# Kernel optimization log

Measured on AMD Instinct MI355X. Metric: run time of the kernel, lower is better.

The kernel has to match this reference:

```python
import jax, jax.numpy as jnp
import numpy as np

K = 20          # num neighbors (init kwarg k)
BN_EPS = 1e-5   # PyTorch BatchNorm default eps


def setup_inputs() -> dict:
    key = jax.random.key(0)
    k1, k2 = jax.random.split(key, 2)
    x = jax.random.normal(k1, (8, 64, 4096), dtype=jnp.float32)       # (b, d, n)
    w = jax.random.normal(k2, (64, 128), dtype=jnp.float32) * 0.05    # Conv2d 1x1: (out=64, in=2*64)
    gamma = jnp.ones((64,), jnp.float32)    # BatchNorm1d weight
    beta = jnp.zeros((64,), jnp.float32)    # BatchNorm1d bias
    return {"x": x, "w": w, "gamma": gamma, "beta": beta}


def reference(x, w, gamma, beta):
    # x: (b, d, n)
    xt = jnp.swapaxes(x, 1, 2)                       # (b, n, d)
    # kNN via pairwise squared euclidean distance (same ordering as torch.cdist)
    sq = jnp.sum(xt * xt, axis=-1)                   # (b, n)
    d2 = sq[:, :, None] + sq[:, None, :] - 2.0 * jnp.einsum('bnd,bmd->bnm', xt, xt)
    _, idx = jax.lax.top_k(-d2, K)                   # (b, n, K) smallest distances
    # gather neighbor features: (b, n, K, d)
    nb = jax.vmap(lambda pts, i: pts[i])(xt, idx)
    ctr = xt[:, :, None, :]                          # (b, n, 1, d)
    # edge feature = concat([neighbor - x, x]) -> (b, n, K, 2d)
    feat = jnp.concatenate([nb - ctr, jnp.broadcast_to(ctr, nb.shape)], axis=-1)
    # 1x1 conv (no bias) then max over neighbors
    h = jnp.max(jnp.einsum('bnkc,oc->bnko', feat, w), axis=2)   # (b, n, out)
    # BatchNorm1d (training mode: batch statistics over (b, n), biased var)
    mean = jnp.mean(h, axis=(0, 1))
    var = jnp.mean((h - mean) ** 2, axis=(0, 1))
    hn = (h - mean) / jnp.sqrt(var + BN_EPS) * gamma + beta
    out = jax.nn.gelu(hn, approximate=False)         # exact GELU (PyTorch default)
    return jnp.swapaxes(out, 1, 2)                   # (b, out, n)
```

## Files before the change

### kernel.cpp

```cpp
#include <hip/hip_runtime.h>

#define BIGF 3.402823466e38f

typedef __attribute__((ext_vector_type(8))) short bf16x8;
typedef __attribute__((ext_vector_type(4))) float f32x4;

__device__ __forceinline__ void gload_lds16(const float* g, float* lds) {
  __builtin_amdgcn_global_load_lds((const __attribute__((address_space(1))) void*)g,
                                   (__attribute__((address_space(3))) void*)lds, 16, 0, 0);
}
__device__ __forceinline__ void gload_lds16u(const unsigned short* g, unsigned short* lds) {
  __builtin_amdgcn_global_load_lds((const __attribute__((address_space(1))) void*)g,
                                   (__attribute__((address_space(3))) void*)lds, 16, 0, 0);
}

__device__ __forceinline__ unsigned short bf16_rne(float f) {
  unsigned int u = __float_as_uint(f);
  return (unsigned short)((u + 0x7fffu + ((u >> 16) & 1u)) >> 16);
}

__global__ __launch_bounds__(256) void k1_pre(const float* __restrict__ x, const float* __restrict__ w,
                                              float* __restrict__ sq, float* __restrict__ y,
                                              float* __restrict__ delta, unsigned short* __restrict__ xhl) {
  __shared__ __align__(16) float xt[64][68];
  __shared__ __align__(16) float ws[128][64];
  const int t = threadIdx.x;
  const int bid = blockIdx.x;
  const int b = bid >> 6;
  const int n0 = (bid & 63) << 6;
  const float* xb = x + (size_t)b * 64 * 4096;

#pragma unroll
  for (int rep = 0; rep < 16; ++rep) {
    int id = rep * 256 + t;
    int d = id >> 6, n = id & 63;
    xt[n][d] = xb[(size_t)d * 4096 + n0 + n];
  }
#pragma unroll
  for (int rep = 0; rep < 32; ++rep) {
    int id = rep * 256 + t;
    int u = id >> 6, dd = id & 63;
    ws[u][dd] = w[(u & 63) * 128 + ((u >> 6) << 6) + dd];
  }
  __syncthreads();

  {
    const int p = t >> 2;
    const int cg = t & 3;
    uint4* orow = (uint4*)xhl + ((size_t)(b << 12) + n0 + p) * 16;
#pragma unroll
    for (int cc = 0; cc < 4; ++cc) {
      const int c = cg * 4 + cc;
      const int kb = (c & 7) * 8;
      const bool lohalf = (c >= 8);
      unsigned int pk[4];
#pragma unroll
      for (int j2 = 0; j2 < 4; ++j2) {
        unsigned short u0, u1;
#pragma unroll
        for (int e = 0; e < 2; ++e) {
          const float xv = xt[p][kb + j2 * 2 + e];
          unsigned short h = bf16_rne(xv);
          unsigned short r;
          if (!lohalf) r = h;
          else r = bf16_rne(xv - __uint_as_float(((unsigned int)h) << 16));
          if (e == 0) u0 = r; else u1 = r;
        }
        pk[j2] = (unsigned int)u0 | ((unsigned int)u1 << 16);
      }
      uint4 v;
      v.x = pk[0]; v.y = pk[1]; v.z = pk[2]; v.w = pk[3];
      orow[c ^ (p & 7)] = v;
    }
  }

  const int p = t & 63;
  const int oc = t >> 6;
  float accy[16], accz[16];
#pragma unroll
  for (int j = 0; j < 16; ++j) { accy[j] = 0.f; accz[j] = 0.f; }

#pragma unroll 4
  for (int d4 = 0; d4 < 16; ++d4) {
    const float4 xv = *(const float4*)&xt[p][d4 * 4];
#pragma unroll
    for (int j = 0; j < 16; ++j) {
      const int o = oc * 16 + j;
      const float4 wy = *(const float4*)&ws[o][d4 * 4];
      const float4 wz = *(const float4*)&ws[o + 64][d4 * 4];
      accy[j] = fmaf(xv.x, wy.x, fmaf(xv.y, wy.y, fmaf(xv.z, wy.z, fmaf(xv.w, wy.w, accy[j]))));
      accz[j] = fmaf(xv.x, wz.x, fmaf(xv.y, wz.y, fmaf(xv.z, wz.z, fmaf(xv.w, wz.w, accz[j]))));
    }
  }

  if (oc == 0) {
    float s = 0.f;
#pragma unroll
    for (int d4 = 0; d4 < 16; ++d4) {
      const float4 v = *(const float4*)&xt[p][d4 * 4];
      s = fmaf(v.x, v.x, fmaf(v.y, v.y, fmaf(v.z, v.z, fmaf(v.w, v.w, s))));
    }
    sq[b * 4096 + n0 + p] = s;
  }

  const size_t row = ((size_t)b * 4096 + n0 + p) * 64 + oc * 16;
#pragma unroll
  for (int j4 = 0; j4 < 4; ++j4) {
    float4 yv = make_float4(accy[j4 * 4], accy[j4 * 4 + 1], accy[j4 * 4 + 2], accy[j4 * 4 + 3]);
    float4 dv = make_float4(accz[j4 * 4] - accy[j4 * 4], accz[j4 * 4 + 1] - accy[j4 * 4 + 1],
                            accz[j4 * 4 + 2] - accy[j4 * 4 + 2], accz[j4 * 4 + 3] - accy[j4 * 4 + 3]);
    *(float4*)&y[row + j4 * 4] = yv;
    *(float4*)&delta[row + j4 * 4] = dv;
  }
}

__global__ __launch_bounds__(256, 2) void k2_knn(const unsigned short* __restrict__ xhl,
                                                 const float* __restrict__ sq,
                                                 int* __restrict__ idx_out) {
  __shared__ __align__(16) float smem[4096 + 8192 + 6656];
  const int t = threadIdx.x;
  const int lane = t & 63;
  const int w = t >> 6;
  float* BsW = smem + 4096 + (w << 11);
  uint4* BsW4 = (uint4*)BsW;
  const uint4* As4 = (const uint4*)smem;
  uint2* bufL = (uint2*)(smem + 12288) + ((w << 6) + lane) * 13;

  const int bid = blockIdx.x;
  const int b = bid >> 6;
  const int n0 = (bid & 63) << 6;
  const int pn = lane & 15, q = lane >> 4;

  const unsigned short* xr = xhl + ((size_t)(b << 12)) * 128;
  const float* sqb = sq + (b << 12);

  {
    unsigned short* asu = (unsigned short*)smem;
#pragma unroll
    for (int qq = 0; qq < 4; ++qq) {
      const int kk = w * 4 + qq;
      gload_lds16u(xr + (size_t)n0 * 128 + kk * 512 + lane * 8, asu + kk * 512);
    }
  }
  __syncthreads();

  bf16x8 bfr[4][4];
#pragma unroll
  for (int nt = 0; nt < 4; ++nt)
#pragma unroll
    for (int j = 0; j < 4; ++j)
      bfr[nt][j] = *reinterpret_cast<const bf16x8*>(&As4[((nt << 4) + pn) * 16 + (((j << 2) + q) ^ (pn & 7))]);

  float kd[20];
  int ki[20];
#pragma unroll
  for (int s = 0; s < 20; ++s) { kd[s] = BIGF; ki[s] = -1; }
  const float sqn = sqb[n0 + lane];
  const int myn = lane;
  const int swz = myn & 7;
  int cnt = 0;

  auto ins = [&](float vd, int vi) {
#pragma unroll
    for (int s = 0; s < 20; ++s) {
      const float od = kd[s];
      const int oi = ki[s];
      const bool lt = vd < od;
      kd[s] = lt ? vd : od;
      ki[s] = lt ? vi : oi;
      vd = lt ? od : vd;
      vi = lt ? oi : vi;
    }
  };

  auto drain = [&]() {
#pragma unroll 1
    for (int j = 0; j < 12; ++j) {
      if (!__any(j < cnt)) break;
      if (j < cnt) {
        const uint2 e = bufL[j];
        const float dv = __uint_as_float(e.x);
        if (dv < kd[19]) ins(dv, (int)e.y);
      }
    }
    cnt = 0;
  };

  const f32x4 zero4 = {0.f, 0.f, 0.f, 0.f};
  f32x4 acc[4][2];
#pragma unroll
  for (int nt = 0; nt < 4; ++nt) { acc[nt][0] = zero4; acc[nt][1] = zero4; }

  for (int kt = 0; kt < 32; ++kt) {
    const int mbase = (w + 4 * kt) << 5;
    {
      unsigned short* bsu = (unsigned short*)BsW;
      const unsigned short* src = xr + (size_t)mbase * 128;
#pragma unroll
      for (int k = 0; k < 8; ++k) gload_lds16u(src + k * 512 + lane * 8, bsu + k * 512);
    }
    const f32x4 sqm0 = *(const f32x4*)&sqb[mbase + (q << 2)];
    const f32x4 sqm1 = *(const f32x4*)&sqb[mbase + 16 + (q << 2)];
    __builtin_amdgcn_s_waitcnt(0x0F70);

#pragma unroll
    for (int mt = 0; mt < 2; ++mt) {
      bf16x8 afr[4];
#pragma unroll
      for (int j = 0; j < 4; ++j)
        afr[j] = *reinterpret_cast<const bf16x8*>(&BsW4[((mt << 4) + pn) * 16 + (((j << 2) + q) ^ (pn & 7))]);
#pragma unroll
      for (int nt = 0; nt < 4; ++nt) {
        f32x4 a = acc[nt][mt];
        a = __builtin_amdgcn_mfma_f32_16x16x32_bf16(afr[0], bfr[nt][0], a, 0, 0, 0);
        a = __builtin_amdgcn_mfma_f32_16x16x32_bf16(afr[1], bfr[nt][1], a, 0, 0, 0);
        a = __builtin_amdgcn_mfma_f32_16x16x32_bf16(afr[0], bfr[nt][2], a, 0, 0, 0);
        a = __builtin_amdgcn_mfma_f32_16x16x32_bf16(afr[1], bfr[nt][3], a, 0, 0, 0);
        a = __builtin_amdgcn_mfma_f32_16x16x32_bf16(afr[2], bfr[nt][0], a, 0, 0, 0);
        a = __builtin_amdgcn_mfma_f32_16x16x32_bf16(afr[3], bfr[nt][1], a, 0, 0, 0);
        acc[nt][mt] = a;
      }
    }

#pragma unroll
    for (int nt = 0; nt < 4; ++nt) {
#pragma unroll
      for (int mt = 0; mt < 2; ++mt) {
        const int n = (nt << 4) + pn;
        const int g = (mt << 2) + q;
        const int pc = g ^ (n & 7);
        const f32x4 sv = mt ? sqm1 : sqm0;
        f32x4 dv = sv - 2.0f * acc[nt][mt];
        *(f32x4*)&BsW[(n << 5) + (pc << 2)] = dv;
        acc[nt][mt] = zero4;
      }
    }

#pragma unroll 1
    for (int cc = 0; cc < 8; ++cc) {
      const float4 v = *(const float4*)&BsW[(myn << 5) + ((cc ^ swz) << 2)];
      const int mb = mbase + (cc << 2);
      const float c0 = sqn + v.x, c1 = sqn + v.y, c2 = sqn + v.z, c3 = sqn + v.w;
      const float thr = kd[19];
      const float mn = fminf(fminf(c0, c1), fminf(c2, c3));
      if (mn < thr) {
        if (c0 < thr) { bufL[cnt] = make_uint2(__float_as_uint(c0), (unsigned)mb); cnt++; }
        if (c1 < thr) { bufL[cnt] = make_uint2(__float_as_uint(c1), (unsigned)(mb + 1)); cnt++; }
        if (c2 < thr) { bufL[cnt] = make_uint2(__float_as_uint(c2), (unsigned)(mb + 2)); cnt++; }
        if (c3 < thr) { bufL[cnt] = make_uint2(__float_as_uint(c3), (unsigned)(mb + 3)); cnt++; }
      }
      if (__any(cnt > 8)) drain();
    }
  }
  drain();

  __syncthreads();
  float* pf = smem;
  int* pi = (int*)(smem + 5120);
#pragma unroll
  for (int s = 0; s < 20; ++s) {
    pf[(w * 20 + s) * 64 + lane] = kd[s];
    pi[(w * 20 + s) * 64 + lane] = ki[s];
  }
  __syncthreads();
  if (w == 0) {
    auto insTie = [&](float vd, int vi) {
#pragma unroll
      for (int s = 0; s < 20; ++s) {
        const float od = kd[s];
        const int oi = ki[s];
        const bool lt = (vd < od) || (vd == od && vi < oi);
        kd[s] = lt ? vd : od;
        ki[s] = lt ? vi : oi;
        vd = lt ? od : vd;
        vi = lt ? oi : vi;
      }
    };
    for (int ww = 1; ww < 4; ++ww) {
#pragma unroll 1
      for (int s = 0; s < 20; ++s) {
        const float dv = pf[(ww * 20 + s) * 64 + lane];
        const int iv = pi[(ww * 20 + s) * 64 + lane];
        if (dv < kd[19] || (dv == kd[19] && iv < ki[19])) insTie(dv, iv);
      }
    }
    int* orow = idx_out + ((size_t)(b << 12) + n0 + lane) * 20;
#pragma unroll
    for (int s = 0; s < 20; ++s) orow[s] = ki[s];
  }
}

__global__ __launch_bounds__(256) void k3_gather(const float* __restrict__ y,
                                                 const float* __restrict__ delta,
                                                 const int* __restrict__ idx,
                                                 float* __restrict__ h,
                                                 float* __restrict__ sums,
                                                 float* __restrict__ sumsq) {
  const int t = threadIdx.x;
  const int lane = t & 63;
  const int w = t >> 6;
  const int blk = blockIdx.x;
  float s1 = 0.f, s2 = 0.f;
  for (int p = 0; p < 16; ++p) {
    const int ng = blk * 64 + w * 16 + p;
    const int b = ng >> 12;
    const int* row = idx + (size_t)ng * 20;
    float mx = -BIGF;
#pragma unroll
    for (int kk = 0; kk < 20; ++kk) {
      const int nbr = row[kk];
      mx = fmaxf(mx, y[((size_t)(b << 12) + nbr) * 64 + lane]);
    }
    const float hv = mx + delta[(size_t)ng * 64 + lane];
    h[(size_t)ng * 64 + lane] = hv;
    s1 += hv;
    s2 += hv * hv;
  }
  __shared__ float r1[4][64], r2[4][64];
  r1[w][lane] = s1;
  r2[w][lane] = s2;
  __syncthreads();
  if (w == 0) {
    const float a = r1[0][lane] + r1[1][lane] + r1[2][lane] + r1[3][lane];
    const float c = r2[0][lane] + r2[1][lane] + r2[2][lane] + r2[3][lane];
    atomicAdd(&sums[lane], a);
    atomicAdd(&sumsq[lane], c);
  }
}

__global__ __launch_bounds__(256) void k4_bn(const float* __restrict__ h,
                                             const float* __restrict__ sums,
                                             const float* __restrict__ sumsq,
                                             const float* __restrict__ gamma,
                                             const float* __restrict__ beta,
                                             float* __restrict__ out) {
  __shared__ float tile[64][65];
  const int bid = blockIdx.x;
  const int b = bid >> 6;
  const int n0 = (bid & 63) << 6;
  const int t = threadIdx.x;
  const int o = t & 63;
#pragma unroll
  for (int it = 0; it < 16; ++it) {
    const int n = (t >> 6) * 16 + it;
    tile[n][o] = h[(((size_t)b << 12) + n0 + n) * 64 + o];
  }
  __syncthreads();
  const int j = t & 63;
#pragma unroll
  for (int it = 0; it < 16; ++it) {
    const int oo = (t >> 6) * 16 + it;
    const float mean = sums[oo] * (1.0f / 32768.0f);
    const float var = sumsq[oo] * (1.0f / 32768.0f) - mean * mean;
    const float sc = gamma[oo] / sqrtf(var + 1e-5f);
    const float hv = tile[j][oo];
    const float hn = (hv - mean) * sc + beta[oo];
    const float g = 0.5f * hn * (1.0f + erff(hn * 0.70710678118654752f));
    out[((size_t)(b * 64 + oo)) * 4096 + n0 + j] = g;
  }
}

extern "C" void kernel_launch(void* const* d_in, const int* in_sizes, int n_in,
                              void* d_out, int out_size, void* d_ws, size_t ws_size,
                              hipStream_t stream) {
  const float* x = (const float*)d_in[0];
  const float* w = (const float*)d_in[1];
  const float* gamma = (const float*)d_in[2];
  const float* beta = (const float*)d_in[3];
  float* out = (float*)d_out;

  float* sq_ws = (float*)d_ws;
  float* y_ws = sq_ws + 32768;
  float* delta_ws = y_ws + 2097152;
  float* h_ws = delta_ws + 2097152;
  int* idx_ws = (int*)(h_ws + 2097152);
  float* sums = (float*)(idx_ws + 655360);
  float* sumsq = sums + 64;
  unsigned short* xhl = (unsigned short*)h_ws;

  hipMemsetAsync(sums, 0, 2 * 64 * sizeof(float), stream);
  k1_pre<<<512, 256, 0, stream>>>(x, w, sq_ws, y_ws, delta_ws, xhl);
  k2_knn<<<512, 256, 0, stream>>>(xhl, sq_ws, idx_ws);
  k3_gather<<<512, 256, 0, stream>>>(y_ws, delta_ws, idx_ws, h_ws, sums, sumsq);
  k4_bn<<<512, 256, 0, stream>>>(h_ws, sums, sumsq, gamma, beta, out);
}
```

Before: 346.6 us.

## Share per-query kNN thresholds across waves and hoist candidate filter loads

Each wave publishes its current 20th-best distance per query point to shared memory after draining. At each tile the waves read all four thresholds and filter candidates against the minimum plus a margin, so fewer candidates are pushed into the buffer and insertion-sorted. The filter now compares raw LDS values against a precomputed threshold minus the query norm, and the four float4 loads for each half are issued together. The cost is extra LDS traffic through volatile accesses, and the cross-wave reads are unsynchronised, so a wave may see a stale threshold.

```diff
diff --git a/kernel.cpp b/kernel.cpp
--- a/kernel.cpp
+++ b/kernel.cpp
@@ -117,7 +117,7 @@
 __global__ __launch_bounds__(256, 2) void k2_knn(const unsigned short* __restrict__ xhl,
                                                  const float* __restrict__ sq,
                                                  int* __restrict__ idx_out) {
-  __shared__ __align__(16) float smem[4096 + 8192 + 6656];
+  __shared__ __align__(16) float smem[4096 + 8192 + 6656 + 256];
   const int t = threadIdx.x;
   const int lane = t & 63;
   const int w = t >> 6;
@@ -125,6 +125,7 @@
   uint4* BsW4 = (uint4*)BsW;
   const uint4* As4 = (const uint4*)smem;
   uint2* bufL = (uint2*)(smem + 12288) + ((w << 6) + lane) * 13;
+  volatile float* thrW = smem + 18944;
 
   const int bid = blockIdx.x;
   const int b = bid >> 6;
@@ -133,6 +134,8 @@
 
   const unsigned short* xr = xhl + ((size_t)(b << 12)) * 128;
   const float* sqb = sq + (b << 12);
+
+  thrW[t] = BIGF;
 
   {
     unsigned short* asu = (unsigned short*)smem;
@@ -184,6 +187,7 @@
       }
     }
     cnt = 0;
+    thrW[(myn << 2) + w] = kd[19];
   };
 
   const f32x4 zero4 = {0.f, 0.f, 0.f, 0.f};
@@ -201,6 +205,15 @@
     }
     const f32x4 sqm0 = *(const f32x4*)&sqb[mbase + (q << 2)];
     const f32x4 sqm1 = *(const f32x4*)&sqb[mbase + 16 + (q << 2)];
+
+    const float tw0 = thrW[(myn << 2) + 0];
+    const float tw1 = thrW[(myn << 2) + 1];
+    const float tw2 = thrW[(myn << 2) + 2];
+    const float tw3 = thrW[(myn << 2) + 3];
+    float thrS = fminf(fminf(tw0, tw1), fminf(tw2, tw3));
+    thrS = fminf(thrS, kd[19]);
+    const float thr2 = (thrS - sqn) + 0.0625f;
+
     __builtin_amdgcn_s_waitcnt(0x0F70);
 
 #pragma unroll
@@ -237,19 +250,25 @@
     }
 
 #pragma unroll 1
-    for (int cc = 0; cc < 8; ++cc) {
-      const float4 v = *(const float4*)&BsW[(myn << 5) + ((cc ^ swz) << 2)];
-      const int mb = mbase + (cc << 2);
-      const float c0 = sqn + v.x, c1 = sqn + v.y, c2 = sqn + v.z, c3 = sqn + v.w;
-      const float thr = kd[19];
-      const float mn = fminf(fminf(c0, c1), fminf(c2, c3));
-      if (mn < thr) {
-        if (c0 < thr) { bufL[cnt] = make_uint2(__float_as_uint(c0), (unsigned)mb); cnt++; }
-        if (c1 < thr) { bufL[cnt] = make_uint2(__float_as_uint(c1), (unsigned)(mb + 1)); cnt++; }
-        if (c2 < thr) { bufL[cnt] = make_uint2(__float_as_uint(c2), (unsigned)(mb + 2)); cnt++; }
-        if (c3 < thr) { bufL[cnt] = make_uint2(__float_as_uint(c3), (unsigned)(mb + 3)); cnt++; }
-      }
-      if (__any(cnt > 8)) drain();
+    for (int half = 0; half < 2; ++half) {
+      const int cb = half << 2;
+      const float4 v0 = *(const float4*)&BsW[(myn << 5) + (((cb + 0) ^ swz) << 2)];
+      const float4 v1 = *(const float4*)&BsW[(myn << 5) + (((cb + 1) ^ swz) << 2)];
+      const float4 v2 = *(const float4*)&BsW[(myn << 5) + (((cb + 2) ^ swz) << 2)];
+      const float4 v3 = *(const float4*)&BsW[(myn << 5) + (((cb + 3) ^ swz) << 2)];
+#pragma unroll
+      for (int cc = 0; cc < 4; ++cc) {
+        const float4 v = (cc == 0) ? v0 : (cc == 1) ? v1 : (cc == 2) ? v2 : v3;
+        const int mb = mbase + ((cb + cc) << 2);
+        const float mn = fminf(fminf(v.x, v.y), fminf(v.z, v.w));
+        if (mn < thr2) {
+          if (v.x < thr2) { bufL[cnt] = make_uint2(__float_as_uint(sqn + v.x), (unsigned)mb); cnt++; }
+          if (v.y < thr2) { bufL[cnt] = make_uint2(__float_as_uint(sqn + v.y), (unsigned)(mb + 1)); cnt++; }
+          if (v.z < thr2) { bufL[cnt] = make_uint2(__float_as_uint(sqn + v.z), (unsigned)(mb + 2)); cnt++; }
+          if (v.w < thr2) { bufL[cnt] = make_uint2(__float_as_uint(sqn + v.w), (unsigned)(mb + 3)); cnt++; }
+        }
+        if (__any(cnt > 8)) drain();
+      }
     }
   }
   drain();
```

New measurement: 344.2 us. No clear change (-0.7%).

## Retile kNN kernel to 32 queries per block with shared threshold and prefetch

Applied to the files above, without the earlier changes.

The kNN kernel now processes 32 query points per block instead of 64, launching 1024 blocks at up to 3 blocks per CU with a smaller LDS footprint. Each candidate tile is 16 points, loaded asynchronously one iteration ahead. Two lanes split candidates per query and then merge. A per-query threshold in shared memory, lowered by atomicMin, lets all waves prune candidates early. The threshold test is done before adding sqn, with a small 0.0625 margin. This trades higher occupancy and pruning for smaller MFMA tiles, more atomics, and a larger final merge.

```diff
diff --git a/kernel.cpp b/kernel.cpp
--- a/kernel.cpp
+++ b/kernel.cpp
@@ -5,10 +5,6 @@
 typedef __attribute__((ext_vector_type(8))) short bf16x8;
 typedef __attribute__((ext_vector_type(4))) float f32x4;
 
-__device__ __forceinline__ void gload_lds16(const float* g, float* lds) {
-  __builtin_amdgcn_global_load_lds((const __attribute__((address_space(1))) void*)g,
-                                   (__attribute__((address_space(3))) void*)lds, 16, 0, 0);
-}
 __device__ __forceinline__ void gload_lds16u(const unsigned short* g, unsigned short* lds) {
   __builtin_amdgcn_global_load_lds((const __attribute__((address_space(1))) void*)g,
                                    (__attribute__((address_space(3))) void*)lds, 16, 0, 0);
@@ -114,50 +110,65 @@
   }
 }
 
-__global__ __launch_bounds__(256, 2) void k2_knn(const unsigned short* __restrict__ xhl,
+__global__ __launch_bounds__(256, 3) void k2_knn(const unsigned short* __restrict__ xhl,
                                                  const float* __restrict__ sq,
                                                  int* __restrict__ idx_out) {
-  __shared__ __align__(16) float smem[4096 + 8192 + 6656];
+  __shared__ __align__(16) float smem[10784];
   const int t = threadIdx.x;
   const int lane = t & 63;
   const int w = t >> 6;
-  float* BsW = smem + 4096 + (w << 11);
-  uint4* BsW4 = (uint4*)BsW;
+  const int bid = blockIdx.x;
+  const int b = bid & 7;
+  const int n0 = (bid >> 3) << 5;
+  const int pn = lane & 15, q = lane >> 4;
+  const int myn = lane & 31;
+  const int h = lane >> 5;
+
+  float* dumpW = smem + (w << 9);
+  float* stW = smem + 2048 + (w << 10);
   const uint4* As4 = (const uint4*)smem;
-  uint2* bufL = (uint2*)(smem + 12288) + ((w << 6) + lane) * 13;
-
-  const int bid = blockIdx.x;
-  const int b = bid >> 6;
-  const int n0 = (bid & 63) << 6;
-  const int pn = lane & 15, q = lane >> 4;
+  const uint4* St4 = (const uint4*)stW;
+  uint2* bufL = (uint2*)(smem + 6144) + t * 9;
+  unsigned* thrNa = (unsigned*)(smem + 10752);
+  volatile unsigned* thrNv = (volatile unsigned*)(smem + 10752);
 
   const unsigned short* xr = xhl + ((size_t)(b << 12)) * 128;
   const float* sqb = sq + (b << 12);
 
+  if (t < 32) thrNa[t] = __float_as_uint(BIGF);
+
   {
     unsigned short* asu = (unsigned short*)smem;
 #pragma unroll
-    for (int qq = 0; qq < 4; ++qq) {
-      const int kk = w * 4 + qq;
+    for (int qq = 0; qq < 2; ++qq) {
+      const int kk = (w << 1) + qq;
       gload_lds16u(xr + (size_t)n0 * 128 + kk * 512 + lane * 8, asu + kk * 512);
     }
   }
-  __syncthreads();
-
-  bf16x8 bfr[4][4];
-#pragma unroll
-  for (int nt = 0; nt < 4; ++nt)
+  {
+    unsigned short* stu = (unsigned short*)stW;
+    const unsigned short* src = xr + (size_t)(w << 4) * 128;
+#pragma unroll
+    for (int k = 0; k < 4; ++k) gload_lds16u(src + k * 512 + lane * 8, stu + k * 512);
+  }
+  f32x4 sqm = *(const f32x4*)&sqb[(w << 4) + (q << 2)];
+  __builtin_amdgcn_s_waitcnt(0x0F70);
+  __syncthreads();
+
+  bf16x8 bfr[2][4];
+#pragma unroll
+  for (int nt = 0; nt < 2; ++nt)
 #pragma unroll
     for (int j = 0; j < 4; ++j)
       bfr[nt][j] = *reinterpret_cast<const bf16x8*>(&As4[((nt << 4) + pn) * 16 + (((j << 2) + q) ^ (pn & 7))]);
+  __syncthreads();
 
   float kd[20];
   int ki[20];
 #pragma unroll
   for (int s = 0; s < 20; ++s) { kd[s] = BIGF; ki[s] = -1; }
-  const float sqn = sqb[n0 + lane];
-  const int myn = lane;
-  const int swz = myn & 7;
+  const float sqn = sqb[n0 + myn];
+  const int fdw = (myn >> 1) & 3;
   int cnt = 0;
 
   auto ins = [&](float vd, int vi) {
@@ -175,7 +186,7 @@
 
   auto drain = [&]() {
 #pragma unroll 1
-    for (int j = 0; j < 12; ++j) {
+    for (int j = 0; j < 8; ++j) {
       if (!__any(j < cnt)) break;
       if (j < cnt) {
         const uint2 e = bufL[j];
@@ -184,73 +195,74 @@
       }
     }
     cnt = 0;
+    atomicMin(&thrNa[myn], __float_as_uint(kd[19]));
   };
 
   const f32x4 zero4 = {0.f, 0.f, 0.f, 0.f};
-  f32x4 acc[4][2];
-#pragma unroll
-  for (int nt = 0; nt < 4; ++nt) { acc[nt][0] = zero4; acc[nt][1] = zero4; }
-
-  for (int kt = 0; kt < 32; ++kt) {
-    const int mbase = (w + 4 * kt) << 5;
-    {
-      unsigned short* bsu = (unsigned short*)BsW;
-      const unsigned short* src = xr + (size_t)mbase * 128;
-#pragma unroll
-      for (int k = 0; k < 8; ++k) gload_lds16u(src + k * 512 + lane * 8, bsu + k * 512);
-    }
-    const f32x4 sqm0 = *(const f32x4*)&sqb[mbase + (q << 2)];
-    const f32x4 sqm1 = *(const f32x4*)&sqb[mbase + 16 + (q << 2)];
+  f32x4 acc[2];
+  acc[0] = zero4; acc[1] = zero4;
+  f32x4 sqmN = zero4;
+
+  for (int kt = 0; kt < 64; ++kt) {
+    const int mbase = (w + (kt << 2)) << 4;
     __builtin_amdgcn_s_waitcnt(0x0F70);
 
-#pragma unroll
-    for (int mt = 0; mt < 2; ++mt) {
-      bf16x8 afr[4];
-#pragma unroll
-      for (int j = 0; j < 4; ++j)
-        afr[j] = *reinterpret_cast<const bf16x8*>(&BsW4[((mt << 4) + pn) * 16 + (((j << 2) + q) ^ (pn & 7))]);
-#pragma unroll
-      for (int nt = 0; nt < 4; ++nt) {
-        f32x4 a = acc[nt][mt];
-        a = __builtin_amdgcn_mfma_f32_16x16x32_bf16(afr[0], bfr[nt][0], a, 0, 0, 0);
-        a = __builtin_amdgcn_mfma_f32_16x16x32_bf16(afr[1], bfr[nt][1], a, 0, 0, 0);
-        a = __builtin_amdgcn_mfma_f32_16x16x32_bf16(afr[0], bfr[nt][2], a, 0, 0, 0);
-        a = __builtin_amdgcn_mfma_f32_16x16x32_bf16(afr[1], bfr[nt][3], a, 0, 0, 0);
-        a = __builtin_amdgcn_mfma_f32_16x16x32_bf16(afr[2], bfr[nt][0], a, 0, 0, 0);
-        a = __builtin_amdgcn_mfma_f32_16x16x32_bf16(afr[3], bfr[nt][1], a, 0, 0, 0);
-        acc[nt][mt] = a;
+    const float thrSh = __uint_as_float(thrNv[myn]);
+    const float thrS = fminf(thrSh, kd[19]);
+    const float thr2 = (thrS - sqn) + 0.0625f;
+
+    bf16x8 afr[4];
+#pragma unroll
+    for (int j = 0; j < 4; ++j)
+      afr[j] = *reinterpret_cast<const bf16x8*>(&St4[pn * 16 + (((j << 2) + q) ^ (pn & 7))]);
+    __builtin_amdgcn_s_waitcnt(0xC07F);
+
+    if (kt < 63) {
+      const int mbn = (w + ((kt + 1) << 2)) << 4;
+      unsigned short* stu = (unsigned short*)stW;
+      const unsigned short* src = xr + (size_t)mbn * 128;
+#pragma unroll
+      for (int k = 0; k < 4; ++k) gload_lds16u(src + k * 512 + lane * 8, stu + k * 512);
+      sqmN = *(const f32x4*)&sqb[mbn + (q << 2)];
+    }
+
+#pragma unroll
+    for (int nt = 0; nt < 2; ++nt) {
+      f32x4 a = acc[nt];
+      a = __builtin_amdgcn_mfma_f32_16x16x32_bf16(afr[0], bfr[nt][0], a, 0, 0, 0);
+      a = __builtin_amdgcn_mfma_f32_16x16x32_bf16(afr[1], bfr[nt][1], a, 0, 0, 0);
+      a = __builtin_amdgcn_mfma_f32_16x16x32_bf16(afr[0], bfr[nt][2], a, 0, 0, 0);
+      a = __builtin_amdgcn_mfma_f32_16x16x32_bf16(afr[1], bfr[nt][3], a, 0, 0, 0);
+      a = __builtin_amdgcn_mfma_f32_16x16x32_bf16(afr[2], bfr[nt][0], a, 0, 0, 0);
+      a = __builtin_amdgcn_mfma_f32_16x16x32_bf16(afr[3], bfr[nt][1], a, 0, 0, 0);
+      acc[nt] = a;
+    }
+
+#pragma unroll
+    for (int nt = 0; nt < 2; ++nt) {
+      const int n = (nt << 4) + pn;
+      const int pc = q ^ ((n >> 1) & 3);
+      f32x4 dv = sqm - 2.0f * acc[nt];
+      *(f32x4*)&dumpW[(n << 4) + (pc << 2)] = dv;
+      acc[nt] = zero4;
+    }
+
+#pragma unroll 1
+    for (int cc2 = 0; cc2 < 2; ++cc2) {
+      const int cc = (h << 1) + cc2;
+      const int pc = cc ^ fdw;
+      const float4 v = *(const float4*)&dumpW[(myn << 4) + (pc << 2)];
+      const int mb = mbase + (cc << 2);
+      const float mn = fminf(fminf(v.x, v.y), fminf(v.z, v.w));
+      if (mn < thr2) {
+        if (v.x < thr2) { bufL[cnt] = make_uint2(__float_as_uint(sqn + v.x), (unsigned)mb); cnt++; }
+        if (v.y < thr2) { bufL[cnt] = make_uint2(__float_as_uint(sqn + v.y), (unsigned)(mb + 1)); cnt++; }
+        if (v.z < thr2) { bufL[cnt] = make_uint2(__float_as_uint(sqn + v.z), (unsigned)(mb + 2)); cnt++; }
+        if (v.w < thr2) { bufL[cnt] = make_uint2(__float_as_uint(sqn + v.w), (unsigned)(mb + 3)); cnt++; }
       }
-    }
-
-#pragma unroll
-    for (int nt = 0; nt < 4; ++nt) {
-#pragma unroll
-      for (int mt = 0; mt < 2; ++mt) {
-        const int n = (nt << 4) + pn;
-        const int g = (mt << 2) + q;
-        const int pc = g ^ (n & 7);
-        const f32x4 sv = mt ? sqm1 : sqm0;
-        f32x4 dv = sv - 2.0f * acc[nt][mt];
-        *(f32x4*)&BsW[(n << 5) + (pc << 2)] = dv;
-        acc[nt][mt] = zero4;
-      }
-    }
-
-#pragma unroll 1
-    for (int cc = 0; cc < 8; ++cc) {
-      const float4 v = *(const float4*)&BsW[(myn << 5) + ((cc ^ swz) << 2)];
-      const int mb = mbase + (cc << 2);
-      const float c0 = sqn + v.x, c1 = sqn + v.y, c2 = sqn + v.z, c3 = sqn + v.w;
-      const float thr = kd[19];
-      const float mn = fminf(fminf(c0, c1), fminf(c2, c3));
-      if (mn < thr) {
-        if (c0 < thr) { bufL[cnt] = make_uint2(__float_as_uint(c0), (unsigned)mb); cnt++; }
-        if (c1 < thr) { bufL[cnt] = make_uint2(__float_as_uint(c1), (unsigned)(mb + 1)); cnt++; }
-        if (c2 < thr) { bufL[cnt] = make_uint2(__float_as_uint(c2), (unsigned)(mb + 2)); cnt++; }
-        if (c3 < thr) { bufL[cnt] = make_uint2(__float_as_uint(c3), (unsigned)(mb + 3)); cnt++; }
-      }
-      if (__any(cnt > 8)) drain();
-    }
+      if (__any(cnt > 4)) drain();
+    }
+    sqm = sqmN;
   }
   drain();
 
@@ -263,7 +275,7 @@
     pi[(w * 20 + s) * 64 + lane] = ki[s];
   }
   __syncthreads();
-  if (w == 0) {
+  if (w == 0 && lane < 32) {
     auto insTie = [&](float vd, int vi) {
 #pragma unroll
       for (int s = 0; s < 20; ++s) {
@@ -276,15 +288,19 @@
         vi = lt ? oi : vi;
       }
     };
-    for (int ww = 1; ww < 4; ++ww) {
+    for (int ww = 0; ww < 4; ++ww) {
 #pragma unroll 1
-      for (int s = 0; s < 20; ++s) {
-        const float dv = pf[(ww * 20 + s) * 64 + lane];
-        const int iv = pi[(ww * 20 + s) * 64 + lane];
-        if (dv < kd[19] || (dv == kd[19] && iv < ki[19])) insTie(dv, iv);
+      for (int hh = 0; hh < 2; ++hh) {
+        if (ww == 0 && hh == 0) continue;
+#pragma unroll 1
+        for (int s = 0; s < 20; ++s) {
+          const float dv = pf[(ww * 20 + s) * 64 + (hh << 5) + myn];
+          const int iv = pi[(ww * 20 + s) * 64 + (hh << 5) + myn];
+          if (dv < kd[19] || (dv == kd[19] && iv < ki[19])) insTie(dv, iv);
+        }
       }
     }
-    int* orow = idx_out + ((size_t)(b << 12) + n0 + lane) * 20;
+    int* orow = idx_out + ((size_t)(b << 12) + n0 + myn) * 20;
 #pragma unroll
     for (int s = 0; s < 20; ++s) orow[s] = ki[s];
   }
@@ -380,7 +396,7 @@
 
   hipMemsetAsync(sums, 0, 2 * 64 * sizeof(float), stream);
   k1_pre<<<512, 256, 0, stream>>>(x, w, sq_ws, y_ws, delta_ws, xhl);
-  k2_knn<<<512, 256, 0, stream>>>(xhl, sq_ws, idx_ws);
+  k2_knn<<<1024, 256, 0, stream>>>(xhl, sq_ws, idx_ws);
   k3_gather<<<512, 256, 0, stream>>>(y_ws, delta_ws, idx_ws, h_ws, sums, sumsq);
   k4_bn<<<512, 256, 0, stream>>>(h_ws, sums, sumsq, gamma, beta, out);
 }
```

Measured after the change: 504.0 us. 1.45x slower.

## Prefetch next kNN tile, share per-query threshold across waves, shrink candidate buffers

Applied to the files above, without the earlier changes.

Restructures the kNN distance loop so the next key tile and its squared norms are loaded into LDS while the current tile's MFMA and selection run. A per-query threshold shared across the four waves, kept in LDS and tightened with atomicMin after each drain, is used so fewer candidates pass the filter. The candidate buffer moves to a struct-of-arrays layout in reused LDS, and the dump tile is halved to 16 columns per half-tile. Risks include extra LDS atomics, a slack margin of 0.0625 on the threshold, and a subtle race in reusing the A-tile LDS region for the buffers, which is guarded by an added barrier.

```diff
diff --git a/kernel.cpp b/kernel.cpp
--- a/kernel.cpp
+++ b/kernel.cpp
@@ -5,10 +5,6 @@
 typedef __attribute__((ext_vector_type(8))) short bf16x8;
 typedef __attribute__((ext_vector_type(4))) float f32x4;
 
-__device__ __forceinline__ void gload_lds16(const float* g, float* lds) {
-  __builtin_amdgcn_global_load_lds((const __attribute__((address_space(1))) void*)g,
-                                   (__attribute__((address_space(3))) void*)lds, 16, 0, 0);
-}
 __device__ __forceinline__ void gload_lds16u(const unsigned short* g, unsigned short* lds) {
   __builtin_amdgcn_global_load_lds((const __attribute__((address_space(1))) void*)g,
                                    (__attribute__((address_space(3))) void*)lds, 16, 0, 0);
@@ -117,31 +113,46 @@
 __global__ __launch_bounds__(256, 2) void k2_knn(const unsigned short* __restrict__ xhl,
                                                  const float* __restrict__ sq,
                                                  int* __restrict__ idx_out) {
-  __shared__ __align__(16) float smem[4096 + 8192 + 6656];
+  __shared__ __align__(16) float smem[16448];
   const int t = threadIdx.x;
   const int lane = t & 63;
   const int w = t >> 6;
-  float* BsW = smem + 4096 + (w << 11);
-  uint4* BsW4 = (uint4*)BsW;
+  float* stW = smem + 4096 + (w << 11);
+  float* dumpW = smem + 12288 + (w << 10);
   const uint4* As4 = (const uint4*)smem;
-  uint2* bufL = (uint2*)(smem + 12288) + ((w << 6) + lane) * 13;
+  const uint4* St4 = (const uint4*)stW;
+  unsigned* bufD = (unsigned*)smem;
+  unsigned* bufI = (unsigned*)(smem + 2048);
+  unsigned* thrNa = (unsigned*)(smem + 16384);
+  volatile unsigned* thrNv = (volatile unsigned*)(smem + 16384);
 
   const int bid = blockIdx.x;
   const int b = bid >> 6;
   const int n0 = (bid & 63) << 6;
   const int pn = lane & 15, q = lane >> 4;
+  const int myn = lane;
 
   const unsigned short* xr = xhl + ((size_t)(b << 12)) * 128;
   const float* sqb = sq + (b << 12);
 
+  if (t < 64) thrNa[t] = 0x7F7FFFFFu;
+
   {
     unsigned short* asu = (unsigned short*)smem;
 #pragma unroll
     for (int qq = 0; qq < 4; ++qq) {
-      const int kk = w * 4 + qq;
+      const int kk = (w << 2) + qq;
       gload_lds16u(xr + (size_t)n0 * 128 + kk * 512 + lane * 8, asu + kk * 512);
     }
-  }
+    unsigned short* stu = (unsigned short*)stW;
+    const unsigned short* src = xr + (size_t)(w << 5) * 128;
+#pragma unroll
+    for (int k = 0; k < 8; ++k) gload_lds16u(src + k * 512 + lane * 8, stu + k * 512);
+  }
+  f32x4 sqm0 = *(const f32x4*)&sqb[(w << 5) + (q << 2)];
+  f32x4 sqm1 = *(const f32x4*)&sqb[(w << 5) + 16 + (q << 2)];
+  const float sqn = sqb[n0 + myn];
+  __builtin_amdgcn_s_waitcnt(0x0F70);
   __syncthreads();
 
   bf16x8 bfr[4][4];
@@ -150,14 +161,13 @@
 #pragma unroll
     for (int j = 0; j < 4; ++j)
       bfr[nt][j] = *reinterpret_cast<const bf16x8*>(&As4[((nt << 4) + pn) * 16 + (((j << 2) + q) ^ (pn & 7))]);
+  __syncthreads();
 
   float kd[20];
   int ki[20];
 #pragma unroll
   for (int s = 0; s < 20; ++s) { kd[s] = BIGF; ki[s] = -1; }
-  const float sqn = sqb[n0 + lane];
-  const int myn = lane;
-  const int swz = myn & 7;
+  const int swz = myn & 3;
   int cnt = 0;
 
   auto ins = [&](float vd, int vi) {
@@ -175,82 +185,99 @@
 
   auto drain = [&]() {
 #pragma unroll 1
-    for (int j = 0; j < 12; ++j) {
+    for (int j = 0; j < 8; ++j) {
       if (!__any(j < cnt)) break;
       if (j < cnt) {
-        const uint2 e = bufL[j];
-        const float dv = __uint_as_float(e.x);
-        if (dv < kd[19]) ins(dv, (int)e.y);
+        const float dv = __uint_as_float(bufD[j * 256 + t]);
+        const int iv = (int)bufI[j * 256 + t];
+        if (dv < kd[19]) ins(dv, iv);
       }
     }
     cnt = 0;
+    atomicMin(&thrNa[myn], __float_as_uint(kd[19]));
   };
 
   const f32x4 zero4 = {0.f, 0.f, 0.f, 0.f};
   f32x4 acc[4][2];
 #pragma unroll
   for (int nt = 0; nt < 4; ++nt) { acc[nt][0] = zero4; acc[nt][1] = zero4; }
+  f32x4 sqmN0 = zero4, sqmN1 = zero4;
 
   for (int kt = 0; kt < 32; ++kt) {
-    const int mbase = (w + 4 * kt) << 5;
-    {
-      unsigned short* bsu = (unsigned short*)BsW;
-      const unsigned short* src = xr + (size_t)mbase * 128;
-#pragma unroll
-      for (int k = 0; k < 8; ++k) gload_lds16u(src + k * 512 + lane * 8, bsu + k * 512);
-    }
-    const f32x4 sqm0 = *(const f32x4*)&sqb[mbase + (q << 2)];
-    const f32x4 sqm1 = *(const f32x4*)&sqb[mbase + 16 + (q << 2)];
+    const int mbase = (w + (kt << 2)) << 5;
     __builtin_amdgcn_s_waitcnt(0x0F70);
 
+    const float thrSh = __uint_as_float(thrNv[myn]);
+    const float thrS = fminf(thrSh, kd[19]);
+    const float thr2 = (thrS - sqn) + 0.0625f;
+
+    bf16x8 afr0[4], afr1[4];
+#pragma unroll
+    for (int j = 0; j < 4; ++j)
+      afr0[j] = *reinterpret_cast<const bf16x8*>(&St4[pn * 16 + (((j << 2) + q) ^ (pn & 7))]);
+#pragma unroll
+    for (int j = 0; j < 4; ++j)
+      afr1[j] = *reinterpret_cast<const bf16x8*>(&St4[(16 + pn) * 16 + (((j << 2) + q) ^ (pn & 7))]);
+    __builtin_amdgcn_s_waitcnt(0xC07F);
+
+    if (kt < 31) {
+      const int mbn = (w + ((kt + 1) << 2)) << 5;
+      unsigned short* stu = (unsigned short*)stW;
+      const unsigned short* src = xr + (size_t)mbn * 128;
+#pragma unroll
+      for (int k = 0; k < 8; ++k) gload_lds16u(src + k * 512 + lane * 8, stu + k * 512);
+      sqmN0 = *(const f32x4*)&sqb[mbn + (q << 2)];
+      sqmN1 = *(const f32x4*)&sqb[mbn + 16 + (q << 2)];
+    }
+
+#pragma unroll
+    for (int nt = 0; nt < 4; ++nt) {
+      f32x4 a = acc[nt][0];
+      a = __builtin_amdgcn_mfma_f32_16x16x32_bf16(afr0[0], bfr[nt][0], a, 0, 0, 0);
+      a = __builtin_amdgcn_mfma_f32_16x16x32_bf16(afr0[1], bfr[nt][1], a, 0, 0, 0);
+      a = __builtin_amdgcn_mfma_f32_16x16x32_bf16(afr0[0], bfr[nt][2], a, 0, 0, 0);
+      a = __builtin_amdgcn_mfma_f32_16x16x32_bf16(afr0[1], bfr[nt][3], a, 0, 0, 0);
+      a = __builtin_amdgcn_mfma_f32_16x16x32_bf16(afr0[2], bfr[nt][0], a, 0, 0, 0);
+      a = __builtin_amdgcn_mfma_f32_16x16x32_bf16(afr0[3], bfr[nt][1], a, 0, 0, 0);
+      acc[nt][0] = a;
+      f32x4 c = acc[nt][1];
+      c = __builtin_amdgcn_mfma_f32_16x16x32_bf16(afr1[0], bfr[nt][0], c, 0, 0, 0);
+      c = __builtin_amdgcn_mfma_f32_16x16x32_bf16(afr1[1], bfr[nt][1], c, 0, 0, 0);
+      c = __builtin_amdgcn_mfma_f32_16x16x32_bf16(afr1[0], bfr[nt][2], c, 0, 0, 0);
+      c = __builtin_amdgcn_mfma_f32_16x16x32_bf16(afr1[1], bfr[nt][3], c, 0, 0, 0);
+      c = __builtin_amdgcn_mfma_f32_16x16x32_bf16(afr1[2], bfr[nt][0], c, 0, 0, 0);
+      c = __builtin_amdgcn_mfma_f32_16x16x32_bf16(afr1[3], bfr[nt][1], c, 0, 0, 0);
+      acc[nt][1] = c;
+    }
+
 #pragma unroll
     for (int mt = 0; mt < 2; ++mt) {
-      bf16x8 afr[4];
-#pragma unroll
-      for (int j = 0; j < 4; ++j)
-        afr[j] = *reinterpret_cast<const bf16x8*>(&BsW4[((mt << 4) + pn) * 16 + (((j << 2) + q) ^ (pn & 7))]);
+      const f32x4 sv = mt ? sqm1 : sqm0;
 #pragma unroll
       for (int nt = 0; nt < 4; ++nt) {
-        f32x4 a = acc[nt][mt];
-        a = __builtin_amdgcn_mfma_f32_16x16x32_bf16(afr[0], bfr[nt][0], a, 0, 0, 0);
-        a = __builtin_amdgcn_mfma_f32_16x16x32_bf16(afr[1], bfr[nt][1], a, 0, 0, 0);
-        a = __builtin_amdgcn_mfma_f32_16x16x32_bf16(afr[0], bfr[nt][2], a, 0, 0, 0);
-        a = __builtin_amdgcn_mfma_f32_16x16x32_bf16(afr[1], bfr[nt][3], a, 0, 0, 0);
-        a = __builtin_amdgcn_mfma_f32_16x16x32_bf16(afr[2], bfr[nt][0], a, 0, 0, 0);
-        a = __builtin_amdgcn_mfma_f32_16x16x32_bf16(afr[3], bfr[nt][1], a, 0, 0, 0);
-        acc[nt][mt] = a;
-      }
-    }
-
-#pragma unroll
-    for (int nt = 0; nt < 4; ++nt) {
-#pragma unroll
-      for (int mt = 0; mt < 2; ++mt) {
         const int n = (nt << 4) + pn;
-        const int g = (mt << 2) + q;
-        const int pc = g ^ (n & 7);
-        const f32x4 sv = mt ? sqm1 : sqm0;
+        const int pc = q ^ (n & 3);
         f32x4 dv = sv - 2.0f * acc[nt][mt];
-        *(f32x4*)&BsW[(n << 5) + (pc << 2)] = dv;
+        *(f32x4*)&dumpW[(n << 4) + (pc << 2)] = dv;
         acc[nt][mt] = zero4;
       }
-    }
-
+      const int mb0 = mbase + (mt << 4);
 #pragma unroll 1
-    for (int cc = 0; cc < 8; ++cc) {
-      const float4 v = *(const float4*)&BsW[(myn << 5) + ((cc ^ swz) << 2)];
-      const int mb = mbase + (cc << 2);
-      const float c0 = sqn + v.x, c1 = sqn + v.y, c2 = sqn + v.z, c3 = sqn + v.w;
-      const float thr = kd[19];
-      const float mn = fminf(fminf(c0, c1), fminf(c2, c3));
-      if (mn < thr) {
-        if (c0 < thr) { bufL[cnt] = make_uint2(__float_as_uint(c0), (unsigned)mb); cnt++; }
-        if (c1 < thr) { bufL[cnt] = make_uint2(__float_as_uint(c1), (unsigned)(mb + 1)); cnt++; }
-        if (c2 < thr) { bufL[cnt] = make_uint2(__float_as_uint(c2), (unsigned)(mb + 2)); cnt++; }
-        if (c3 < thr) { bufL[cnt] = make_uint2(__float_as_uint(c3), (unsigned)(mb + 3)); cnt++; }
-      }
-      if (__any(cnt > 8)) drain();
-    }
+      for (int cc = 0; cc < 4; ++cc) {
+        const float4 v = *(const float4*)&dumpW[(myn << 4) + ((cc ^ swz) << 2)];
+        const int mb = mb0 + (cc << 2);
+        const float mn = fminf(fminf(v.x, v.y), fminf(v.z, v.w));
+        if (mn < thr2) {
+          if (v.x < thr2) { bufD[cnt * 256 + t] = __float_as_uint(sqn + v.x); bufI[cnt * 256 + t] = (unsigned)mb; cnt++; }
+          if (v.y < thr2) { bufD[cnt * 256 + t] = __float_as_uint(sqn + v.y); bufI[cnt * 256 + t] = (unsigned)(mb + 1); cnt++; }
+          if (v.z < thr2) { bufD[cnt * 256 + t] = __float_as_uint(sqn + v.z); bufI[cnt * 256 + t] = (unsigned)(mb + 2); cnt++; }
+          if (v.w < thr2) { bufD[cnt * 256 + t] = __float_as_uint(sqn + v.w); bufI[cnt * 256 + t] = (unsigned)(mb + 3); cnt++; }
+        }
+        if (__any(cnt > 4)) drain();
+      }
+    }
+    sqm0 = sqmN0;
+    sqm1 = sqmN1;
   }
   drain();
 
```

Result: slower. 358.3 us (+3.4%).
